# Kernel tuning notes

Hardware: AMD Instinct MI355X
Metric: run time of the kernel (lower is better)

## Reference

```python
import jax, jax.numpy as jnp
import numpy as np

N, E, B, DIN, D = 65536, 1048576, 256, 32, 64
NUM_STEPS_MP = 2   # num_step_message_passing
SET2SET_STEPS = 3  # processing_steps
NUM_CLASSES = 4


def setup_inputs() -> dict:
    key = jax.random.key(0)
    ks = jax.random.split(key, 24)
    def gl(k, shape, fan_in):
        return (jax.random.normal(k, shape, jnp.float32) / np.sqrt(fan_in)).astype(jnp.float32)
    x = jax.random.normal(ks[0], (N, DIN), jnp.float32)
    edge_index = jax.random.randint(ks[1], (2, E), 0, N, dtype=jnp.int32).astype(jnp.int64)
    batch = jnp.sort(jax.random.randint(ks[2], (N,), 0, B, dtype=jnp.int32)).astype(jnp.int64)
    inp = dict(
        x=x, edge_index=edge_index, batch=batch,
        # conv1.mlp: Linear(DIN -> D)
        W_mlp=gl(ks[3], (D, DIN), DIN), b_mlp=jnp.zeros((D,), jnp.float32),
        # HenrionConv linear (D -> D), messages scatter-summed over edges
        W_conv=gl(ks[4], (D, D), D), b_conv=jnp.zeros((D,), jnp.float32),
        # GRU(input = D + DIN, hidden = D); gate order r,z,n (PyTorch)
        gru_W_ih=gl(ks[5], (3 * D, D + DIN), D + DIN),
        gru_W_hh=gl(ks[6], (3 * D, D), D),
        gru_b_ih=jnp.zeros((3 * D,), jnp.float32),
        gru_b_hh=jnp.zeros((3 * D,), jnp.float32),
        # Set2Set LSTM(input = 2D, hidden = D); gate order i,f,g,o (PyTorch)
        lstm_W_ih=gl(ks[7], (4 * D, 2 * D), 2 * D),
        lstm_W_hh=gl(ks[8], (4 * D, D), D),
        lstm_b_ih=jnp.zeros((4 * D,), jnp.float32),
        lstm_b_hh=jnp.zeros((4 * D,), jnp.float32),
        # head MLPs
        W1=gl(ks[9], (D, 2 * D), 2 * D), b1=jnp.zeros((D,), jnp.float32),
        W2=gl(ks[10], (NUM_CLASSES, D), D), b2=jnp.zeros((NUM_CLASSES,), jnp.float32),
        num_graphs=B,
    )
    return inp


def _forward(x, edge_index, batch, W_mlp, b_mlp, W_conv, b_conv,
             gru_W_ih, gru_W_hh, gru_b_ih, gru_b_hh,
             lstm_W_ih, lstm_W_hh, lstm_b_ih, lstm_b_hh,
             W1, b1, W2, b2, num_graphs):
    n = x.shape[0]
    d = W_mlp.shape[0]
    src, dst = edge_index[0], edge_index[1]

    # ---- Henrion_MPNNConv ----
    out = x @ W_mlp.T + b_mlp            # [N, D]
    h = out
    for _ in range(NUM_STEPS_MP):
        # HenrionConv: linear on source node features, scatter-sum to destinations
        msg = (out @ W_conv.T + b_conv)[src]               # [E, D] gather
        m = jax.ops.segment_sum(msg, dst, num_segments=n)  # [N, D] scatter
        inp = jnp.concatenate([m, x], axis=-1)             # [N, D+DIN]
        # GRU cell (seq len 1)
        gi = inp @ gru_W_ih.T + gru_b_ih
        gh = h @ gru_W_hh.T + gru_b_hh
        gi_r, gi_z, gi_n = jnp.split(gi, 3, axis=-1)
        gh_r, gh_z, gh_n = jnp.split(gh, 3, axis=-1)
        r = jax.nn.sigmoid(gi_r + gh_r)
        z = jax.nn.sigmoid(gi_z + gh_z)
        ng = jnp.tanh(gi_n + r * gh_n)
        h = (1.0 - z) * ng + z * h
        out = h

    # ---- Set2Set (processing_steps = 3) ----
    bsz = num_graphs
    q_star = jnp.zeros((bsz, 2 * d), out.dtype)
    hl = jnp.zeros((bsz, d), out.dtype)
    cl = jnp.zeros((bsz, d), out.dtype)
    for _ in range(SET2SET_STEPS):
        gates = q_star @ lstm_W_ih.T + lstm_b_ih + hl @ lstm_W_hh.T + lstm_b_hh
        gi, gf, gg, go = jnp.split(gates, 4, axis=-1)
        cl = jax.nn.sigmoid(gf) * cl + jax.nn.sigmoid(gi) * jnp.tanh(gg)
        hl = jax.nn.sigmoid(go) * jnp.tanh(cl)
        q = hl                                             # [B, D]
        e = jnp.sum(out * q[batch], axis=-1)               # [N]
        e_max = jax.ops.segment_max(e, batch, num_segments=bsz)
        e_max = jnp.where(jnp.isfinite(e_max), e_max, 0.0)
        a = jnp.exp(e - e_max[batch])
        a_sum = jax.ops.segment_sum(a, batch, num_segments=bsz)
        a = a / jnp.maximum(a_sum[batch], 1e-16)           # segment softmax
        r = jax.ops.segment_sum(a[:, None] * out, batch, num_segments=bsz)  # [B, D]
        q_star = jnp.concatenate([q, r], axis=-1)          # [B, 2D]

    # ---- head (eval mode: dropout is identity) ----
    hid = jax.nn.relu(q_star @ W1.T + b1)
    logits = hid @ W2.T + b2
    return jax.nn.log_softmax(logits, axis=-1)             # [B, 4]


def reference(x, edge_index, batch, W_mlp, b_mlp, W_conv, b_conv,
              gru_W_ih, gru_W_hh, gru_b_ih, gru_b_hh,
              lstm_W_ih, lstm_W_hh, lstm_b_ih, lstm_b_hh,
              W1, b1, W2, b2, num_graphs):
    return _forward(x, edge_index, batch, W_mlp, b_mlp, W_conv, b_conv,
                    gru_W_ih, gru_W_hh, gru_b_ih, gru_b_hh,
                    lstm_W_ih, lstm_W_hh, lstm_b_ih, lstm_b_hh,
                    W1, b1, W2, b2, num_graphs)
```

## Files before the change

kernel.cpp:

```cpp
#include <hip/hip_runtime.h>
#include <math.h>

constexpr int Nn  = 65536;
constexpr int Ne  = 1048576;
constexpr int Bg  = 256;
constexpr int DIN = 32;
constexpr int D   = 64;

constexpr int NB   = 256;
constexpr int BCAP = 6144;

typedef __attribute__((ext_vector_type(8))) short bf16x8;
typedef __attribute__((ext_vector_type(8))) unsigned short u16x8;
typedef __attribute__((ext_vector_type(4))) float f32x4;

__device__ __forceinline__ float sigf(float x) { return 1.0f / (1.0f + expf(-x)); }

__device__ __forceinline__ unsigned short bf16_rne(float f) {
  unsigned u = __float_as_uint(f);
  unsigned r = u + 0x7FFFu + ((u >> 16) & 1u);
  return (unsigned short)(r >> 16);
}
__device__ __forceinline__ float bf16_tof(unsigned short h) {
  return __uint_as_float(((unsigned)h) << 16);
}
__device__ __forceinline__ void split2(float f, unsigned short& hi, unsigned short& lo) {
  hi = bf16_rne(f);
  lo = bf16_rne(f - bf16_tof(hi));
}
__device__ __forceinline__ float recon(unsigned short hi, unsigned short lo) {
  return bf16_tof(hi) + bf16_tof(lo);
}

#define MFMA(a, b, c) __builtin_amdgcn_mfma_f32_16x16x32_bf16(a, b, c, 0, 0, 0)

__global__ void k_prepw(const float* __restrict__ W_mlp, const float* __restrict__ W_conv,
                        const float* __restrict__ gWih, const float* __restrict__ gWhh,
                        const float* __restrict__ b_conv,
                        const float* __restrict__ lW_ih, const float* __restrict__ lW_hh,
                        const float* __restrict__ W1,
                        unsigned short* __restrict__ mlp_h, unsigned short* __restrict__ mlp_l,
                        unsigned short* __restrict__ gw_h,  unsigned short* __restrict__ gw_l,
                        float* __restrict__ WihT, float* __restrict__ WhhT,
                        float* __restrict__ W1T, float* __restrict__ vfold,
                        const int* __restrict__ batch, int* __restrict__ gp,
                        int* __restrict__ rp) {
  int idx = blockIdx.x * 256 + threadIdx.x;
  if (idx < 30720) {
    int c = idx / 6144, rem = idx % 6144;
    int nt = rem >> 9, lane = (rem >> 3) & 63, j = rem & 7;
    int n = nt * 16 + (lane & 15);
    int kk = c * 32 + (lane >> 4) * 8 + j;
    float v;
    if (c < 2) {
      float s = 0.f;
      for (int o = 0; o < 64; ++o) s = fmaf(gWih[n * 96 + o], W_conv[o * 64 + kk], s);
      v = s;
    } else if (c == 2) {
      v = gWih[n * 96 + kk];
    } else {
      v = gWhh[n * 64 + (c - 3) * 32 + (lane >> 4) * 8 + j];
    }
    unsigned short hi, lo; split2(v, hi, lo);
    gw_h[idx] = hi; gw_l[idx] = lo;
    return;
  }
  if (idx < 32768) {
    int lp = idx - 30720;
    int nt = lp >> 9, lane = (lp >> 3) & 63, j = lp & 7;
    int n = nt * 16 + (lane & 15);
    unsigned short hi, lo;
    split2(W_mlp[n * 32 + (lane >> 4) * 8 + j], hi, lo);
    mlp_h[lp] = hi; mlp_l[lp] = lo;
    return;
  }
  int t = idx - 32768;
  if (t < 32768) {
    int row = t / 128, k = t % 128;
    WihT[k * 256 + row] = lW_ih[t];
  } else if (t < 49152) {
    int j = t - 32768;
    int row = j / 64, k = j % 64;
    WhhT[k * 256 + row] = lW_hh[j];
  } else if (t < 57344) {
    int j = t - 49152;
    int row = j / 128, k = j % 128;
    W1T[k * 64 + row] = W1[j];
  } else if (t < 57344 + Bg + 1) {
    int g = t - 57344;
    if (g == 0) rp[Nn] = Ne;
    int lo = 0, hi = Nn;
    while (lo < hi) {
      int mid = (lo + hi) >> 1;
      if (batch[mid] < g) lo = mid + 1; else hi = mid;
    }
    gp[g] = lo;
  } else if (t < 57344 + 257 + 192) {
    int g = t - 57344 - 257;
    float s = 0.f;
    for (int o = 0; o < 64; ++o) s = fmaf(gWih[g * 96 + o], b_conv[o], s);
    vfold[g] = s;
  }
}

__global__ __launch_bounds__(256) void k_conv1(const float* __restrict__ x,
                                               const unsigned short* __restrict__ Wh,
                                               const unsigned short* __restrict__ Wl,
                                               const float* __restrict__ bias,
                                               unsigned short* __restrict__ hph,
                                               unsigned short* __restrict__ hpl,
                                               unsigned short* __restrict__ Aih,
                                               unsigned short* __restrict__ Ail) {
  int wave = threadIdx.x >> 6, lane = threadIdx.x & 63;
  int quad = lane >> 4;
  int n0w = blockIdx.x * 64 + wave * 16;
  int rowA = n0w + (lane & 15);
  const float4* xp = (const float4*)&x[(size_t)rowA * 32 + quad * 8];
  float4 xa = xp[0], xb = xp[1];
  float xv[8] = {xa.x, xa.y, xa.z, xa.w, xb.x, xb.y, xb.z, xb.w};
  bf16x8 ah, al;
#pragma unroll
  for (int j = 0; j < 8; ++j) {
    unsigned short hi, lo; split2(xv[j], hi, lo);
    ah[j] = (short)hi; al[j] = (short)lo;
  }
  *(bf16x8*)&Aih[(size_t)rowA * 96 + 64 + quad * 8] = ah;
  *(bf16x8*)&Ail[(size_t)rowA * 96 + 64 + quad * 8] = al;

  f32x4 acc[4] = {};
#pragma unroll
  for (int nt = 0; nt < 4; ++nt) {
    bf16x8 bh = *(const bf16x8*)&Wh[(nt * 64 + lane) * 8];
    bf16x8 bl = *(const bf16x8*)&Wl[(nt * 64 + lane) * 8];
    acc[nt] = MFMA(ah, bh, acc[nt]);
    acc[nt] = MFMA(ah, bl, acc[nt]);
    acc[nt] = MFMA(al, bh, acc[nt]);
  }
  int col0 = lane & 15;
#pragma unroll
  for (int nt = 0; nt < 4; ++nt) {
    float bv = bias[nt * 16 + col0];
#pragma unroll
    for (int r = 0; r < 4; ++r) {
      int node = n0w + quad * 4 + r;
      float v = acc[nt][r] + bv;
      size_t o = (size_t)node * 64 + nt * 16 + col0;
      unsigned short hi, lo; split2(v, hi, lo);
      hph[o] = hi; hpl[o] = lo;
    }
  }
}

__global__ __launch_bounds__(256) void k_aggr(const unsigned short* __restrict__ Hh,
                                              const int* __restrict__ rp,
                                              const int* __restrict__ srcs,
                                              unsigned short* __restrict__ Sh,
                                              unsigned short* __restrict__ Sl) {
  int wave = threadIdx.x >> 6, lane = threadIdx.x & 63;
  int node = blockIdx.x * 4 + wave;
  int s = rp[node], e = rp[node + 1];
  float acc = 0.f;
  for (int base = s; base < e; base += 64) {
    int m = min(64, e - base);
    int idx = (base + lane < e) ? srcs[base + lane] : 0;
    int k = 0;
    for (; k + 4 <= m; k += 4) {
      int s0 = __shfl(idx, k);
      int s1 = __shfl(idx, k + 1);
      int s2 = __shfl(idx, k + 2);
      int s3 = __shfl(idx, k + 3);
      unsigned short v0 = Hh[(size_t)s0 * 64 + lane];
      unsigned short v1 = Hh[(size_t)s1 * 64 + lane];
      unsigned short v2 = Hh[(size_t)s2 * 64 + lane];
      unsigned short v3 = Hh[(size_t)s3 * 64 + lane];
      acc += bf16_tof(v0);
      acc += bf16_tof(v1);
      acc += bf16_tof(v2);
      acc += bf16_tof(v3);
    }
    for (; k < m; ++k) {
      int sk = __shfl(idx, k);
      acc += bf16_tof(Hh[(size_t)sk * 64 + lane]);
    }
  }
  unsigned short hi, lo; split2(acc, hi, lo);
  Sh[(size_t)node * 64 + lane] = hi;
  Sl[(size_t)node * 64 + lane] = lo;
}

__global__ __launch_bounds__(256, 2) void k_gru(const unsigned short* __restrict__ Aih,
                                                const unsigned short* __restrict__ Ail,
                                                const unsigned short* __restrict__ Hh,
                                                const unsigned short* __restrict__ Hl,
                                                const unsigned short* __restrict__ Sh,
                                                const unsigned short* __restrict__ Sl,
                                                const unsigned short* __restrict__ gw_h,
                                                const unsigned short* __restrict__ gw_l,
                                                const float* __restrict__ b_ih,
                                                const float* __restrict__ b_hh,
                                                const float* __restrict__ vfold,
                                                const int* __restrict__ rp,
                                                unsigned short* __restrict__ nph,
                                                unsigned short* __restrict__ npl) {
  __shared__ unsigned short sW[2][12288];
  int tid = threadIdx.x;
  int wave = tid >> 6, lane = tid & 63;
  int quad = lane >> 4;
  int n0w = blockIdx.x * 128 + wave * 32;
  int rowA0 = n0w + (lane & 15);

  f32x4 acc0[12] = {}, acc1[12] = {};
  f32x4 aN0[4] = {}, aN1[4] = {};

  bf16x8 gvh[3], gvl[3];
#pragma unroll
  for (int j = 0; j < 3; ++j) {
    gvh[j] = *(const bf16x8*)&gw_h[(tid + j * 256) * 8];
    gvl[j] = *(const bf16x8*)&gw_l[(tid + j * 256) * 8];
  }
#pragma unroll
  for (int j = 0; j < 3; ++j) {
    *(bf16x8*)&sW[0][(tid + j * 256) * 8] = gvh[j];
    *(bf16x8*)&sW[0][6144 + (tid + j * 256) * 8] = gvl[j];
  }
  __syncthreads();

#pragma unroll
  for (int c = 0; c < 5; ++c) {
    const int buf = c & 1;
    if (c < 4) {
#pragma unroll
      for (int j = 0; j < 3; ++j) {
        gvh[j] = *(const bf16x8*)&gw_h[(c + 1) * 6144 + (tid + j * 256) * 8];
        gvl[j] = *(const bf16x8*)&gw_l[(c + 1) * 6144 + (tid + j * 256) * 8];
      }
    }
    bf16x8 a0h, a0l, a1h, a1l;
    if (c < 2) {
      size_t b0 = (size_t)rowA0 * 64 + c * 32 + quad * 8;
      size_t b1 = (size_t)(rowA0 + 16) * 64 + c * 32 + quad * 8;
      a0h = *(const bf16x8*)&Sh[b0]; a0l = *(const bf16x8*)&Sl[b0];
      a1h = *(const bf16x8*)&Sh[b1]; a1l = *(const bf16x8*)&Sl[b1];
    } else if (c == 2) {
      size_t b0 = (size_t)rowA0 * 96 + 64 + quad * 8;
      size_t b1 = (size_t)(rowA0 + 16) * 96 + 64 + quad * 8;
      a0h = *(const bf16x8*)&Aih[b0]; a0l = *(const bf16x8*)&Ail[b0];
      a1h = *(const bf16x8*)&Aih[b1]; a1l = *(const bf16x8*)&Ail[b1];
    } else {
      size_t b0 = (size_t)rowA0 * 64 + (c - 3) * 32 + quad * 8;
      size_t b1 = (size_t)(rowA0 + 16) * 64 + (c - 3) * 32 + quad * 8;
      a0h = *(const bf16x8*)&Hh[b0]; a0l = *(const bf16x8*)&Hl[b0];
      a1h = *(const bf16x8*)&Hh[b1]; a1l = *(const bf16x8*)&Hl[b1];
    }
    const unsigned short* sw = sW[buf];
#pragma unroll
    for (int nt = 0; nt < 12; ++nt) {
      bf16x8 bh = *(const bf16x8*)&sw[(nt * 64 + lane) * 8];
      bf16x8 bl = *(const bf16x8*)&sw[6144 + (nt * 64 + lane) * 8];
      if (c < 3 || nt < 8) {
        acc0[nt] = MFMA(a0h, bh, acc0[nt]);
        acc0[nt] = MFMA(a0h, bl, acc0[nt]);
        acc0[nt] = MFMA(a0l, bh, acc0[nt]);
        acc1[nt] = MFMA(a1h, bh, acc1[nt]);
        acc1[nt] = MFMA(a1h, bl, acc1[nt]);
        acc1[nt] = MFMA(a1l, bh, acc1[nt]);
      } else {
        aN0[nt - 8] = MFMA(a0h, bh, aN0[nt - 8]);
        aN0[nt - 8] = MFMA(a0h, bl, aN0[nt - 8]);
        aN0[nt - 8] = MFMA(a0l, bh, aN0[nt - 8]);
        aN1[nt - 8] = MFMA(a1h, bh, aN1[nt - 8]);
        aN1[nt - 8] = MFMA(a1h, bl, aN1[nt - 8]);
        aN1[nt - 8] = MFMA(a1l, bh, aN1[nt - 8]);
      }
    }
    if (c < 4) {
#pragma unroll
      for (int j = 0; j < 3; ++j) {
        *(bf16x8*)&sW[1 - buf][(tid + j * 256) * 8] = gvh[j];
        *(bf16x8*)&sW[1 - buf][6144 + (tid + j * 256) * 8] = gvl[j];
      }
    }
    __syncthreads();
  }

  int col0 = lane & 15;
#pragma unroll
  for (int tile = 0; tile < 2; ++tile) {
    int nb = n0w + tile * 16;
#pragma unroll
    for (int r = 0; r < 4; ++r) {
      int node = nb + quad * 4 + r;
      float degf = (float)(rp[node + 1] - rp[node]);
#pragma unroll
      for (int nt = 0; nt < 4; ++nt) {
        int g = nt * 16 + col0;
        size_t o = (size_t)node * 64 + g;
        float br  = b_ih[g] + b_hh[g] + degf * vfold[g];
        float bz  = b_ih[64 + g] + b_hh[64 + g] + degf * vfold[64 + g];
        float bin = b_ih[128 + g] + degf * vfold[128 + g];
        float bhn = b_hh[128 + g];
        float gr = tile ? acc1[nt][r]     : acc0[nt][r];
        float gz = tile ? acc1[nt + 4][r] : acc0[nt + 4][r];
        float gn = tile ? acc1[nt + 8][r] : acc0[nt + 8][r];
        float hn = tile ? aN1[nt][r]      : aN0[nt][r];
        float rr = sigf(gr + br);
        float zz = sigf(gz + bz);
        float nn = tanhf(gn + bin + rr * (hn + bhn));
        float h_old = recon(Hh[o], Hl[o]);
        float hv = (1.f - zz) * nn + zz * h_old;
        unsigned short hi, lo; split2(hv, hi, lo);
        nph[o] = hi; npl[o] = lo;
      }
    }
  }
}

__global__ __launch_bounds__(256) void k_bucket(const int* __restrict__ eidx,
                                                int* __restrict__ gcur,
                                                int* __restrict__ payload) {
  __shared__ int lcnt[NB];
  __shared__ int lcur[NB];
  int t = threadIdx.x;
  int e0 = blockIdx.x * 4096;
  lcnt[t] = 0;
  __syncthreads();
  int ds[16], ss[16];
#pragma unroll
  for (int i = 0; i < 16; ++i) {
    int e = e0 + i * 256 + t;
    ds[i] = eidx[Ne + e];
    ss[i] = eidx[e];
    atomicAdd(&lcnt[ds[i] >> 8], 1);
  }
  __syncthreads();
  lcur[t] = atomicAdd(&gcur[t * 16], lcnt[t]);
  __syncthreads();
#pragma unroll
  for (int i = 0; i < 16; ++i) {
    int b = ds[i] >> 8;
    int p = atomicAdd(&lcur[b], 1);
    if (p < BCAP) payload[b * BCAP + p] = (ss[i] << 8) | (ds[i] & 255);
  }
}

__global__ __launch_bounds__(256) void k_placeB(const int* __restrict__ gcur,
                                                const int* __restrict__ payload,
                                                int* __restrict__ rp,
                                                int* __restrict__ srcs) {
  __shared__ int sAll[NB];
  __shared__ int hst[NB];
  __shared__ int cur[NB];
  int b = blockIdx.x, t = threadIdx.x;
  sAll[t] = gcur[t * 16];
  hst[t] = 0;
  __syncthreads();
  int cnt = min(sAll[b], BCAP);
  for (int off = 1; off < NB; off <<= 1) {
    int v = (t >= off) ? sAll[t - off] : 0;
    __syncthreads();
    sAll[t] += v;
    __syncthreads();
  }
  int base = sAll[b] - gcur[b * 16];
  const int* pay = &payload[b * BCAP];
  for (int i = t; i < cnt; i += 256) atomicAdd(&hst[pay[i] & 255], 1);
  __syncthreads();
  int c = hst[t];
  cur[t] = c;
  __syncthreads();
  for (int off = 1; off < NB; off <<= 1) {
    int v = (t >= off) ? cur[t - off] : 0;
    __syncthreads();
    cur[t] += v;
    __syncthreads();
  }
  int excl = cur[t] - c;
  rp[b * 256 + t] = base + excl;
  cur[t] = base + excl;
  __syncthreads();
  for (int i = t; i < cnt; i += 256) {
    int pl = pay[i];
    int p = atomicAdd(&cur[pl & 255], 1);
    srcs[p] = pl >> 8;
  }
}

constexpr int ACAP = 1024;
__global__ __launch_bounds__(256) void k_s2s(const unsigned short* __restrict__ hph,
                                             const unsigned short* __restrict__ hpl,
                                             const int* __restrict__ gp,
                                             float* __restrict__ q_star,
                                             float* __restrict__ hl,
                                             float* __restrict__ cl,
                                             const float* __restrict__ WihT,
                                             const float* __restrict__ WhhT,
                                             const float* __restrict__ b_ih,
                                             const float* __restrict__ b_hh,
                                             const float* __restrict__ W1T,
                                             const float* __restrict__ b1,
                                             const float* __restrict__ W2,
                                             const float* __restrict__ b2,
                                             float* __restrict__ outp,
                                             int first, int do_head) {
  int g = blockIdx.x;
  int t = threadIdx.x;
  int w = t >> 6, lane = t & 63;
  __shared__ float qs[128], hsh[64], gates[256];
  __shared__ float qsh[64], rsh[64];
  __shared__ float eL[ACAP];
  __shared__ float red[4];
  __shared__ float partial[4][64];
  __shared__ float asum_p[4];
  __shared__ float emax_sh;
  __shared__ float l4[4];

  if (t < 128) qs[t] = first ? 0.f : q_star[g * 128 + t];
  else if (t < 192) hsh[t - 128] = first ? 0.f : hl[g * 64 + (t - 128)];
  __syncthreads();
  {
    float acc = b_ih[t] + b_hh[t];
    for (int k = 0; k < 128; ++k) acc = fmaf(WihT[k * 256 + t], qs[k], acc);
    for (int k = 0; k < 64; ++k)  acc = fmaf(WhhT[k * 256 + t], hsh[k], acc);
    gates[t] = acc;
  }
  __syncthreads();
  if (t < 64) {
    float ig = sigf(gates[t]),        fg = sigf(gates[64 + t]);
    float gg = tanhf(gates[128 + t]), og = sigf(gates[192 + t]);
    float c_old = first ? 0.f : cl[g * 64 + t];
    float c = fg * c_old + ig * gg;
    float q = og * tanhf(c);
    cl[g * 64 + t] = c;
    hl[g * 64 + t] = q;
    q_star[g * 128 + t] = q;
    qsh[t] = q;
  }
  __syncthreads();

  int s = gp[g], e = gp[g + 1];
  int cnt = e - s;

  int c4 = (lane & 15) * 4;
  float4 qv = {qsh[c4], qsh[c4 + 1], qsh[c4 + 2], qsh[c4 + 3]};
  for (int i0 = s + w * 4; i0 < e; i0 += 16) {
    int node = i0 + (lane >> 4);
    float p = 0.f;
    if (node < e) {
      ushort4 h4  = *(const ushort4*)&hph[(size_t)node * 64 + c4];
      ushort4 l4v = *(const ushort4*)&hpl[(size_t)node * 64 + c4];
      p = recon(h4.x, l4v.x) * qv.x + recon(h4.y, l4v.y) * qv.y +
          recon(h4.z, l4v.z) * qv.z + recon(h4.w, l4v.w) * qv.w;
    }
    p += __shfl_xor(p, 1); p += __shfl_xor(p, 2);
    p += __shfl_xor(p, 4); p += __shfl_xor(p, 8);
    if (node < e && (lane & 15) == 0) eL[node - s] = p;
  }
  __syncthreads();

  float m = -INFINITY;
  for (int i = t; i < cnt; i += 256) m = fmaxf(m, eL[i]);
#pragma unroll
  for (int o = 32; o >= 1; o >>= 1) m = fmaxf(m, __shfl_xor(m, o));
  if (lane == 0) red[w] = m;
  __syncthreads();
  if (t == 0) {
    float mm = fmaxf(fmaxf(red[0], red[1]), fmaxf(red[2], red[3]));
    emax_sh = isfinite(mm) ? mm : 0.f;
  }
  __syncthreads();
  float emax = emax_sh;

  float acc = 0.f, asum = 0.f;
  for (int i = s + w; i < e; i += 4) {
    float a = expf(eL[i - s] - emax);
    asum += a;
    float hv = recon(hph[(size_t)i * 64 + lane], hpl[(size_t)i * 64 + lane]);
    acc = fmaf(a, hv, acc);
  }
  partial[w][lane] = acc;
  if (lane == 0) asum_p[w] = asum;
  __syncthreads();
  if (t < 64) {
    float r  = partial[0][t] + partial[1][t] + partial[2][t] + partial[3][t];
    float as = asum_p[0] + asum_p[1] + asum_p[2] + asum_p[3];
    float rv = (cnt > 0) ? r / fmaxf(as, 1e-16f) : 0.f;
    q_star[g * 128 + 64 + t] = rv;
    rsh[t] = rv;
  }
  if (!do_head) return;
  __syncthreads();

  if (t < 64) {
    float a1 = b1[t];
    for (int k = 0; k < 64; ++k)  a1 = fmaf(W1T[k * 64 + t], qsh[k], a1);
    for (int k = 64; k < 128; ++k) a1 = fmaf(W1T[k * 64 + t], rsh[k - 64], a1);
    hsh[t] = fmaxf(a1, 0.f);
  }
  __syncthreads();
  if (t < 4) {
    float lg = b2[t];
    for (int d = 0; d < 64; ++d) lg = fmaf(W2[t * 64 + d], hsh[d], lg);
    l4[t] = lg;
  }
  __syncthreads();
  if (t < 4) {
    float mx = fmaxf(fmaxf(l4[0], l4[1]), fmaxf(l4[2], l4[3]));
    float ssum = expf(l4[0] - mx) + expf(l4[1] - mx) + expf(l4[2] - mx) + expf(l4[3] - mx);
    outp[g * 4 + t] = l4[t] - mx - logf(ssum);
  }
}

extern "C" void kernel_launch(void* const* d_in, const int* in_sizes, int n_in,
                              void* d_out, int out_size, void* d_ws, size_t ws_size,
                              hipStream_t stream) {
  const float* x        = (const float*)d_in[0];
  const int*   eidx     = (const int*)d_in[1];
  const int*   batch    = (const int*)d_in[2];
  const float* W_mlp    = (const float*)d_in[3];
  const float* b_mlp    = (const float*)d_in[4];
  const float* W_conv   = (const float*)d_in[5];
  const float* b_conv   = (const float*)d_in[6];
  const float* gW_ih    = (const float*)d_in[7];
  const float* gW_hh    = (const float*)d_in[8];
  const float* gb_ih    = (const float*)d_in[9];
  const float* gb_hh    = (const float*)d_in[10];
  const float* lW_ih    = (const float*)d_in[11];
  const float* lW_hh    = (const float*)d_in[12];
  const float* lb_ih    = (const float*)d_in[13];
  const float* lb_hh    = (const float*)d_in[14];
  const float* W1       = (const float*)d_in[15];
  const float* b1       = (const float*)d_in[16];
  const float* W2       = (const float*)d_in[17];
  const float* b2       = (const float*)d_in[18];
  float* outp = (float*)d_out;

  char* ws = (char*)d_ws;
  size_t off = 0;
  auto alloc = [&](size_t bytes) { size_t r = off; off = (off + bytes + 255) & ~(size_t)255; return r; };
  unsigned short* hpAh = (unsigned short*)(ws + alloc((size_t)Nn * 64 * 2));
  unsigned short* hpAl = (unsigned short*)(ws + alloc((size_t)Nn * 64 * 2));
  unsigned short* hpBh = (unsigned short*)(ws + alloc((size_t)Nn * 64 * 2));
  unsigned short* hpBl = (unsigned short*)(ws + alloc((size_t)Nn * 64 * 2));
  unsigned short* Aih  = (unsigned short*)(ws + alloc((size_t)Nn * 96 * 2));
  unsigned short* Ail  = (unsigned short*)(ws + alloc((size_t)Nn * 96 * 2));
  unsigned short* Sh   = (unsigned short*)(ws + alloc((size_t)Nn * 64 * 2));
  unsigned short* Sl   = (unsigned short*)(ws + alloc((size_t)Nn * 64 * 2));
  int*   rp    = (int*)(ws + alloc((size_t)(Nn + 1) * 4));
  int*   srcs  = (int*)(ws + alloc((size_t)Ne * 4));
  int*   gcur  = (int*)(ws + alloc((size_t)NB * 16 * 4));
  int*   payload = (int*)(ws + alloc((size_t)NB * BCAP * 4));
  int*   gp    = (int*)(ws + alloc((size_t)(Bg + 1) * 4));
  float* WihT  = (float*)(ws + alloc((size_t)128 * 256 * 4));
  float* WhhT  = (float*)(ws + alloc((size_t)64 * 256 * 4));
  float* W1T   = (float*)(ws + alloc((size_t)128 * 64 * 4));
  float* vfold = (float*)(ws + alloc(192 * 4));
  unsigned short* mlp_h = (unsigned short*)(ws + alloc(2048 * 2));
  unsigned short* mlp_l = (unsigned short*)(ws + alloc(2048 * 2));
  unsigned short* gw_h  = (unsigned short*)(ws + alloc(30720 * 2));
  unsigned short* gw_l  = (unsigned short*)(ws + alloc(30720 * 2));
  float* s2s   = (float*)(ws + alloc((size_t)Bg * (128 + 64 + 64) * 4));
  float* q_star = s2s;
  float* hl     = s2s + Bg * 128;
  float* cl     = s2s + Bg * 128 + Bg * 64;
  (void)in_sizes; (void)n_in; (void)out_size; (void)ws_size;

  hipMemsetAsync(gcur, 0, (size_t)NB * 16 * 4, stream);

  k_bucket<<<Ne / 4096, 256, 0, stream>>>(eidx, gcur, payload);
  k_placeB<<<NB, 256, 0, stream>>>(gcur, payload, rp, srcs);
  k_prepw<<<355, 256, 0, stream>>>(W_mlp, W_conv, gW_ih, gW_hh, b_conv,
                                   lW_ih, lW_hh, W1,
                                   mlp_h, mlp_l, gw_h, gw_l,
                                   WihT, WhhT, W1T, vfold, batch, gp, rp);

  k_conv1<<<Nn / 64, 256, 0, stream>>>(x, mlp_h, mlp_l, b_mlp, hpAh, hpAl, Aih, Ail);

  unsigned short *cph = hpAh, *cpl = hpAl, *nph = hpBh, *npl = hpBl;
  for (int step = 0; step < 2; ++step) {
    k_aggr<<<Nn / 4, 256, 0, stream>>>(cph, rp, srcs, Sh, Sl);
    k_gru<<<Nn / 128, 256, 0, stream>>>(Aih, Ail, cph, cpl, Sh, Sl, gw_h, gw_l,
                                        gb_ih, gb_hh, vfold, rp, nph, npl);
    unsigned short* tu;
    tu = cph; cph = nph; nph = tu;
    tu = cpl; cpl = npl; npl = tu;
  }

  for (int it = 0; it < 3; ++it) {
    k_s2s<<<Bg, 256, 0, stream>>>(cph, cpl, gp, q_star, hl, cl, WihT, WhhT,
                                  lb_ih, lb_hh, W1T, b1, W2, b2, outp,
                                  it == 0 ? 1 : 0, it == 2 ? 1 : 0);
  }
}
```

Before: 323.7 us.

## Fuse Set2Set iterations into one kernel and unroll aggregation gather by eight

The three Set2Set launches are merged into a single kernel per graph that loops over the processing steps, keeping the LSTM state and q_star in shared memory instead of round-tripping through global memory. This removes two launches and the global state traffic. Separately, the edge aggregation gather loop is unrolled from four to eight outstanding loads per wave to raise memory-level parallelism, at some cost in registers.

```diff
diff --git a/kernel.cpp b/kernel.cpp
--- a/kernel.cpp
+++ b/kernel.cpp
@@ -159,28 +159,34 @@
   int wave = threadIdx.x >> 6, lane = threadIdx.x & 63;
   int node = blockIdx.x * 4 + wave;
   int s = rp[node], e = rp[node + 1];
+  int n = e - s;
+  const int* sp = srcs + s;
   float acc = 0.f;
-  for (int base = s; base < e; base += 64) {
-    int m = min(64, e - base);
-    int idx = (base + lane < e) ? srcs[base + lane] : 0;
+  for (int base = 0; base < n; base += 64) {
+    int m = min(64, n - base);
+    int idx = sp[base + ((lane < m) ? lane : 0)];
     int k = 0;
-    for (; k + 4 <= m; k += 4) {
-      int s0 = __shfl(idx, k);
-      int s1 = __shfl(idx, k + 1);
-      int s2 = __shfl(idx, k + 2);
-      int s3 = __shfl(idx, k + 3);
-      unsigned short v0 = Hh[(size_t)s0 * 64 + lane];
-      unsigned short v1 = Hh[(size_t)s1 * 64 + lane];
-      unsigned short v2 = Hh[(size_t)s2 * 64 + lane];
-      unsigned short v3 = Hh[(size_t)s3 * 64 + lane];
-      acc += bf16_tof(v0);
-      acc += bf16_tof(v1);
-      acc += bf16_tof(v2);
-      acc += bf16_tof(v3);
+    for (; k + 8 <= m; k += 8) {
+      int i0 = __shfl(idx, k),     i1 = __shfl(idx, k + 1);
+      int i2 = __shfl(idx, k + 2), i3 = __shfl(idx, k + 3);
+      int i4 = __shfl(idx, k + 4), i5 = __shfl(idx, k + 5);
+      int i6 = __shfl(idx, k + 6), i7 = __shfl(idx, k + 7);
+      unsigned short v0 = Hh[(size_t)i0 * 64 + lane];
+      unsigned short v1 = Hh[(size_t)i1 * 64 + lane];
+      unsigned short v2 = Hh[(size_t)i2 * 64 + lane];
+      unsigned short v3 = Hh[(size_t)i3 * 64 + lane];
+      unsigned short v4 = Hh[(size_t)i4 * 64 + lane];
+      unsigned short v5 = Hh[(size_t)i5 * 64 + lane];
+      unsigned short v6 = Hh[(size_t)i6 * 64 + lane];
+      unsigned short v7 = Hh[(size_t)i7 * 64 + lane];
+      acc += bf16_tof(v0); acc += bf16_tof(v1);
+      acc += bf16_tof(v2); acc += bf16_tof(v3);
+      acc += bf16_tof(v4); acc += bf16_tof(v5);
+      acc += bf16_tof(v6); acc += bf16_tof(v7);
     }
     for (; k < m; ++k) {
-      int sk = __shfl(idx, k);
-      acc += bf16_tof(Hh[(size_t)sk * 64 + lane]);
+      int ik = __shfl(idx, k);
+      acc += bf16_tof(Hh[(size_t)ik * 64 + lane]);
     }
   }
   unsigned short hi, lo; split2(acc, hi, lo);
@@ -389,9 +395,6 @@
 __global__ __launch_bounds__(256) void k_s2s(const unsigned short* __restrict__ hph,
                                              const unsigned short* __restrict__ hpl,
                                              const int* __restrict__ gp,
-                                             float* __restrict__ q_star,
-                                             float* __restrict__ hl,
-                                             float* __restrict__ cl,
                                              const float* __restrict__ WihT,
                                              const float* __restrict__ WhhT,
                                              const float* __restrict__ b_ih,
@@ -400,106 +403,105 @@
                                              const float* __restrict__ b1,
                                              const float* __restrict__ W2,
                                              const float* __restrict__ b2,
-                                             float* __restrict__ outp,
-                                             int first, int do_head) {
+                                             float* __restrict__ outp) {
   int g = blockIdx.x;
   int t = threadIdx.x;
   int w = t >> 6, lane = t & 63;
-  __shared__ float qs[128], hsh[64], gates[256];
-  __shared__ float qsh[64], rsh[64];
+  __shared__ float qstar_s[128];
+  __shared__ float hs[64], cs[64], gates[256];
   __shared__ float eL[ACAP];
   __shared__ float red[4];
   __shared__ float partial[4][64];
   __shared__ float asum_p[4];
   __shared__ float emax_sh;
   __shared__ float l4[4];
-
-  if (t < 128) qs[t] = first ? 0.f : q_star[g * 128 + t];
-  else if (t < 192) hsh[t - 128] = first ? 0.f : hl[g * 64 + (t - 128)];
-  __syncthreads();
-  {
-    float acc = b_ih[t] + b_hh[t];
-    for (int k = 0; k < 128; ++k) acc = fmaf(WihT[k * 256 + t], qs[k], acc);
-    for (int k = 0; k < 64; ++k)  acc = fmaf(WhhT[k * 256 + t], hsh[k], acc);
-    gates[t] = acc;
-  }
-  __syncthreads();
-  if (t < 64) {
-    float ig = sigf(gates[t]),        fg = sigf(gates[64 + t]);
-    float gg = tanhf(gates[128 + t]), og = sigf(gates[192 + t]);
-    float c_old = first ? 0.f : cl[g * 64 + t];
-    float c = fg * c_old + ig * gg;
-    float q = og * tanhf(c);
-    cl[g * 64 + t] = c;
-    hl[g * 64 + t] = q;
-    q_star[g * 128 + t] = q;
-    qsh[t] = q;
-  }
-  __syncthreads();
-
+  __shared__ float hid[64];
+
+  if (t < 128) qstar_s[t] = 0.f;
+  if (t < 64) { hs[t] = 0.f; cs[t] = 0.f; }
   int s = gp[g], e = gp[g + 1];
   int cnt = e - s;
 
-  int c4 = (lane & 15) * 4;
-  float4 qv = {qsh[c4], qsh[c4 + 1], qsh[c4 + 2], qsh[c4 + 3]};
-  for (int i0 = s + w * 4; i0 < e; i0 += 16) {
-    int node = i0 + (lane >> 4);
-    float p = 0.f;
-    if (node < e) {
-      ushort4 h4  = *(const ushort4*)&hph[(size_t)node * 64 + c4];
-      ushort4 l4v = *(const ushort4*)&hpl[(size_t)node * 64 + c4];
-      p = recon(h4.x, l4v.x) * qv.x + recon(h4.y, l4v.y) * qv.y +
-          recon(h4.z, l4v.z) * qv.z + recon(h4.w, l4v.w) * qv.w;
-    }
-    p += __shfl_xor(p, 1); p += __shfl_xor(p, 2);
-    p += __shfl_xor(p, 4); p += __shfl_xor(p, 8);
-    if (node < e && (lane & 15) == 0) eL[node - s] = p;
-  }
-  __syncthreads();
-
-  float m = -INFINITY;
-  for (int i = t; i < cnt; i += 256) m = fmaxf(m, eL[i]);
-#pragma unroll
-  for (int o = 32; o >= 1; o >>= 1) m = fmaxf(m, __shfl_xor(m, o));
-  if (lane == 0) red[w] = m;
-  __syncthreads();
-  if (t == 0) {
-    float mm = fmaxf(fmaxf(red[0], red[1]), fmaxf(red[2], red[3]));
-    emax_sh = isfinite(mm) ? mm : 0.f;
-  }
-  __syncthreads();
-  float emax = emax_sh;
-
-  float acc = 0.f, asum = 0.f;
-  for (int i = s + w; i < e; i += 4) {
-    float a = expf(eL[i - s] - emax);
-    asum += a;
-    float hv = recon(hph[(size_t)i * 64 + lane], hpl[(size_t)i * 64 + lane]);
-    acc = fmaf(a, hv, acc);
-  }
-  partial[w][lane] = acc;
-  if (lane == 0) asum_p[w] = asum;
-  __syncthreads();
-  if (t < 64) {
-    float r  = partial[0][t] + partial[1][t] + partial[2][t] + partial[3][t];
-    float as = asum_p[0] + asum_p[1] + asum_p[2] + asum_p[3];
-    float rv = (cnt > 0) ? r / fmaxf(as, 1e-16f) : 0.f;
-    q_star[g * 128 + 64 + t] = rv;
-    rsh[t] = rv;
-  }
-  if (!do_head) return;
+  for (int it = 0; it < 3; ++it) {
+    __syncthreads();
+
+    {
+      float acc = b_ih[t] + b_hh[t];
+      for (int k = 0; k < 128; ++k) acc = fmaf(WihT[k * 256 + t], qstar_s[k], acc);
+      for (int k = 0; k < 64; ++k)  acc = fmaf(WhhT[k * 256 + t], hs[k], acc);
+      gates[t] = acc;
+    }
+    __syncthreads();
+    if (t < 64) {
+      float ig = sigf(gates[t]),        fg = sigf(gates[64 + t]);
+      float gg = tanhf(gates[128 + t]), og = sigf(gates[192 + t]);
+      float c = fg * cs[t] + ig * gg;
+      float q = og * tanhf(c);
+      cs[t] = c;
+      hs[t] = q;
+      qstar_s[t] = q;
+    }
+    __syncthreads();
+
+    int c4 = (lane & 15) * 4;
+    float4 qv = {qstar_s[c4], qstar_s[c4 + 1], qstar_s[c4 + 2], qstar_s[c4 + 3]};
+    for (int i0 = s + w * 4; i0 < e; i0 += 16) {
+      int node = i0 + (lane >> 4);
+      float p = 0.f;
+      if (node < e) {
+        ushort4 h4  = *(const ushort4*)&hph[(size_t)node * 64 + c4];
+        ushort4 l4v = *(const ushort4*)&hpl[(size_t)node * 64 + c4];
+        p = recon(h4.x, l4v.x) * qv.x + recon(h4.y, l4v.y) * qv.y +
+            recon(h4.z, l4v.z) * qv.z + recon(h4.w, l4v.w) * qv.w;
+      }
+      p += __shfl_xor(p, 1); p += __shfl_xor(p, 2);
+      p += __shfl_xor(p, 4); p += __shfl_xor(p, 8);
+      if (node < e && (lane & 15) == 0) eL[node - s] = p;
+    }
+    __syncthreads();
+
+    float m = -INFINITY;
+    for (int i = t; i < cnt; i += 256) m = fmaxf(m, eL[i]);
+#pragma unroll
+    for (int o = 32; o >= 1; o >>= 1) m = fmaxf(m, __shfl_xor(m, o));
+    if (lane == 0) red[w] = m;
+    __syncthreads();
+    if (t == 0) {
+      float mm = fmaxf(fmaxf(red[0], red[1]), fmaxf(red[2], red[3]));
+      emax_sh = isfinite(mm) ? mm : 0.f;
+    }
+    __syncthreads();
+    float emax = emax_sh;
+
+    float acc = 0.f, asum = 0.f;
+    for (int i = s + w; i < e; i += 4) {
+      float a = expf(eL[i - s] - emax);
+      asum += a;
+      float hv = recon(hph[(size_t)i * 64 + lane], hpl[(size_t)i * 64 + lane]);
+      acc = fmaf(a, hv, acc);
+    }
+    partial[w][lane] = acc;
+    if (lane == 0) asum_p[w] = asum;
+    __syncthreads();
+    if (t < 64) {
+      float r  = partial[0][t] + partial[1][t] + partial[2][t] + partial[3][t];
+      float as = asum_p[0] + asum_p[1] + asum_p[2] + asum_p[3];
+      float rv = (cnt > 0) ? r / fmaxf(as, 1e-16f) : 0.f;
+      qstar_s[64 + t] = rv;
+    }
+  }
   __syncthreads();
 
   if (t < 64) {
     float a1 = b1[t];
-    for (int k = 0; k < 64; ++k)  a1 = fmaf(W1T[k * 64 + t], qsh[k], a1);
-    for (int k = 64; k < 128; ++k) a1 = fmaf(W1T[k * 64 + t], rsh[k - 64], a1);
-    hsh[t] = fmaxf(a1, 0.f);
+    for (int k = 0; k < 64; ++k)   a1 = fmaf(W1T[k * 64 + t], qstar_s[k], a1);
+    for (int k = 64; k < 128; ++k) a1 = fmaf(W1T[k * 64 + t], qstar_s[k], a1);
+    hid[t] = fmaxf(a1, 0.f);
   }
   __syncthreads();
   if (t < 4) {
     float lg = b2[t];
-    for (int d = 0; d < 64; ++d) lg = fmaf(W2[t * 64 + d], hsh[d], lg);
+    for (int d = 0; d < 64; ++d) lg = fmaf(W2[t * 64 + d], hid[d], lg);
     l4[t] = lg;
   }
   __syncthreads();
@@ -558,10 +560,6 @@
   unsigned short* mlp_l = (unsigned short*)(ws + alloc(2048 * 2));
   unsigned short* gw_h  = (unsigned short*)(ws + alloc(30720 * 2));
   unsigned short* gw_l  = (unsigned short*)(ws + alloc(30720 * 2));
-  float* s2s   = (float*)(ws + alloc((size_t)Bg * (128 + 64 + 64) * 4));
-  float* q_star = s2s;
-  float* hl     = s2s + Bg * 128;
-  float* cl     = s2s + Bg * 128 + Bg * 64;
   (void)in_sizes; (void)n_in; (void)out_size; (void)ws_size;
 
   hipMemsetAsync(gcur, 0, (size_t)NB * 16 * 4, stream);
@@ -585,9 +583,6 @@
     tu = cpl; cpl = npl; npl = tu;
   }
 
-  for (int it = 0; it < 3; ++it) {
-    k_s2s<<<Bg, 256, 0, stream>>>(cph, cpl, gp, q_star, hl, cl, WihT, WhhT,
-                                  lb_ih, lb_hh, W1T, b1, W2, b2, outp,
-                                  it == 0 ? 1 : 0, it == 2 ? 1 : 0);
-  }
-}
+  k_s2s<<<Bg, 256, 0, stream>>>(cph, cpl, gp, WihT, WhhT,
+                                lb_ih, lb_hh, W1T, b1, W2, b2, outp);
+}
```

Measured after the change: 363.4 us. 12.2% more time.
